# Kernel tuning notes

Hardware: AMD Instinct MI355X
Metric: run time of the kernel (lower is better)

## Reference

```python
import jax, jax.numpy as jnp
import numpy as np

HID = 1024
EMB = 300
VOCAB = 3863
POSE = 514  # autoencoder_vq_components(512) + 2


def gru_step(h, x, Wih, Whh, bih, bhh):
    # PyTorch GRU cell math. x:[B,Din] h:[B,H] Wih:[3H,Din] Whh:[3H,H]
    gi = x @ Wih.T + bih
    gh = h @ Whh.T + bhh
    i_r, i_z, i_n = jnp.split(gi, 3, axis=-1)
    h_r, h_z, h_n = jnp.split(gh, 3, axis=-1)
    r = jax.nn.sigmoid(i_r + h_r)
    z = jax.nn.sigmoid(i_z + h_z)
    n = jnp.tanh(i_n + r * h_n)
    return (1.0 - z) * n + z * h


def setup_inputs() -> dict:
    key = jax.random.key(0)
    ks = jax.random.split(key, 24)
    s_e = 1.0 / np.sqrt(HID)

    def u(k, shape, scale):
        return jax.random.uniform(k, shape, jnp.float32, -scale, scale)

    inp = {
        # encoder embedding + bidirectional (2 single-direction) GRU weights
        "enc_emb": jax.random.normal(ks[0], (VOCAB, EMB), jnp.float32),
        "enc_Wih_f": u(ks[1], (3 * HID, EMB), s_e),
        "enc_Whh_f": u(ks[2], (3 * HID, HID), s_e),
        "enc_bih_f": u(ks[3], (3 * HID,), s_e),
        "enc_bhh_f": u(ks[4], (3 * HID,), s_e),
        "enc_Wih_b": u(ks[5], (3 * HID, EMB), s_e),
        "enc_Whh_b": u(ks[6], (3 * HID, HID), s_e),
        "enc_bih_b": u(ks[7], (3 * HID,), s_e),
        "enc_bhh_b": u(ks[8], (3 * HID,), s_e),
        # decoder embedding, GRU, output projection
        "dec_emb": jax.random.normal(ks[9], (POSE, HID), jnp.float32),
        "dec_Wih": u(ks[10], (3 * HID, HID), s_e),
        "dec_Whh": u(ks[11], (3 * HID, HID), s_e),
        "dec_bih": u(ks[12], (3 * HID,), s_e),
        "dec_bhh": u(ks[13], (3 * HID,), s_e),
        "fc_W": u(ks[14], (POSE, HID), s_e),
        "fc_b": u(ks[15], (POSE,), s_e),
        # forward args
        "in_text": jax.random.randint(ks[16], (128, 64), 0, VOCAB, jnp.int64 if jax.config.jax_enable_x64 else jnp.int32),
        "in_lengths": jax.random.randint(ks[17], (128,), 1, 64),
        "poses": jax.random.randint(ks[18], (128, 90), 0, POSE),
        "vid_indices": jax.random.randint(ks[19], (128,), 0, 128),
    }
    return inp


def reference(enc_emb, enc_Wih_f, enc_Whh_f, enc_bih_f, enc_bhh_f,
              enc_Wih_b, enc_Whh_b, enc_bih_b, enc_bhh_b,
              dec_emb, dec_Wih, dec_Whh, dec_bih, dec_bhh,
              fc_W, fc_b, in_text, in_lengths, poses, vid_indices):
    B = in_text.shape[0]
    x_emb = enc_emb[in_text.T]  # [T_in, B, 300]
    h0 = jnp.zeros((B, HID), dtype=enc_emb.dtype)

    # The torch code feeds a bidirectional GRU one timestep at a time while
    # carrying hidden state, so BOTH directions act as forward recurrences
    # with their own weights.
    def enc_f(h, xt):
        return gru_step(h, xt, enc_Wih_f, enc_Whh_f, enc_bih_f, enc_bhh_f), None

    def enc_b(h, xt):
        return gru_step(h, xt, enc_Wih_b, enc_Whh_b, enc_bih_b, enc_bhh_b), None

    hf, _ = jax.lax.scan(enc_f, h0, x_emb)
    hb, _ = jax.lax.scan(enc_b, h0, x_emb)
    dec_h0 = hf + hb  # encoder_hidden[:1] + encoder_hidden[1:]

    # Teacher-forcing branch: input at step di is poses[max(di-1, 0)].
    pt = poses.T  # [T_out, B]
    dec_idx = jnp.concatenate([pt[:1], pt[:-1]], axis=0)
    dec_x = dec_emb[dec_idx]  # [T_out, B, HID]

    def dec_step(h, xt):
        h = gru_step(h, xt, dec_Wih, dec_Whh, dec_bih, dec_bhh)
        return h, h

    _, hs = jax.lax.scan(dec_step, dec_h0, dec_x)  # [T_out, B, HID]
    out = jnp.einsum('tbh,oh->tbo', hs, fc_W) + fc_b  # [T_out, B, 514]
    return out
```

## Files before the change

kernel.cpp:

```cpp
#include <hip/hip_runtime.h>
#include <hip/hip_bf16.h>

#define HID   1024
#define G3    3072
#define EMB   300
#define EMBP  320
#define VOCAB 3863
#define POSE  514
#define BATCH 128
#define TIN   64
#define TOUT  90
#define BH    (BATCH * HID)
#define NBLK  256

typedef __bf16 bf16x8 __attribute__((ext_vector_type(8)));
typedef float  f32x4  __attribute__((ext_vector_type(4)));
typedef __hip_bfloat16 bhalf;
typedef unsigned long long u64;

#define MFMA(a,b,c) __builtin_amdgcn_mfma_f32_16x16x32_bf16((a),(b),(c),0,0,0)

__device__ __forceinline__ float sigm(float x) { return 1.f / (1.f + __expf(-x)); }
__device__ __forceinline__ float tanh_f(float x) { return 1.f - 2.f / (__expf(2.f * x) + 1.f); }

#define COH_LD(dst, base, imm)                                            \
  asm volatile("global_load_dwordx4 %0, %1, off offset:%2 sc0 sc1"        \
               : "=v"(dst) : "v"(base), "i"(imm))

__device__ __forceinline__ void coh_st_h(bhalf* p, float v) {
  union { bhalf b; unsigned short s; } u;
  u.b = __float2bfloat16(v);
  __hip_atomic_store((unsigned short*)p, u.s, __ATOMIC_RELAXED, __HIP_MEMORY_SCOPE_AGENT);
}
__device__ __forceinline__ void coh_st_f(float* p, float v) {
  __hip_atomic_store(p, v, __ATOMIC_RELAXED, __HIP_MEMORY_SCOPE_AGENT);
}
__device__ __forceinline__ float coh_ld_f(const float* p) {
  return __hip_atomic_load((const float*)p, __ATOMIC_RELAXED, __HIP_MEMORY_SCOPE_AGENT);
}

__device__ __forceinline__ void gbar(unsigned* bar, unsigned tgt) {
  __syncthreads();
  if (threadIdx.x == 0) {
    __hip_atomic_fetch_add(bar, 1u, __ATOMIC_RELEASE, __HIP_MEMORY_SCOPE_AGENT);
    while (__hip_atomic_load(bar, __ATOMIC_RELAXED, __HIP_MEMORY_SCOPE_AGENT) < tgt)
      __builtin_amdgcn_s_sleep(1);
  }
  __syncthreads();
  asm volatile("" ::: "memory");
}

__global__ void k_zerobar(unsigned* p) {
  int i = blockIdx.x * 256 + threadIdx.x;
  if (i < 1024)
    __hip_atomic_store(p + i, 0u, __ATOMIC_RELAXED, __HIP_MEMORY_SCOPE_AGENT);
}

__global__ __launch_bounds__(256) void k_convert(const float* __restrict__ src,
        bhalf* __restrict__ dst, int rows_in, int cols_in, int cols_out, int total) {
  int i = blockIdx.x * 256 + threadIdx.x;
  if (i >= total) return;
  int r = i / cols_out, c = i - r * cols_out;
  float v = (r < rows_in && c < cols_in) ? src[(size_t)r * cols_in + c] : 0.f;
  dst[i] = __float2bfloat16(v);
}

__global__ __launch_bounds__(256) void k_pack(const float* __restrict__ whh,
                                              bhalf* __restrict__ dst) {
  int i = blockIdx.x * 256 + threadIdx.x;
  if (i >= G3 * HID) return;
  int k  = i & (HID - 1);
  int rp = i >> 10;
  int jg  = rp / 48;
  int rem = rp - jg * 48;
  int g = rem >> 4, jl = rem & 15;
  int j = (jg << 4) + jl;
  dst[i] = __float2bfloat16(whh[(size_t)((g << 10) + j) * HID + k]);
}

template<int OUTBF>
__global__ __launch_bounds__(256) void k_gemm(
    const bhalf* __restrict__ A, const bhalf* __restrict__ B,
    const float* __restrict__ bias, float* __restrict__ Cf, bhalf* __restrict__ Cb,
    int M, int K, int Nstore) {
  int gx = gridDim.x;
  int nwg = gx * gridDim.y;
  int orig = blockIdx.y * gx + blockIdx.x;
  int xcd = orig & 7, sl = orig >> 3;
  int qq = nwg >> 3, rr = nwg & 7;
  int nbid = (xcd < rr ? xcd * (qq + 1) : rr * (qq + 1) + (xcd - rr) * qq) + sl;
  int bx = nbid % gx, by = nbid / gx;

  int tid = threadIdx.x;
  int l = tid & 63, w = tid >> 6;
  int q = l >> 4, jl = l & 15;
  int n0 = bx * 32;
  int m0 = by * 128 + w * 32;
  int ar0 = m0 + jl;       if (ar0 >= M) ar0 = M - 1;
  int ar1 = m0 + 16 + jl;  if (ar1 >= M) ar1 = M - 1;
  const bhalf* pa0 = A + (size_t)ar0 * K + q * 8;
  const bhalf* pa1 = A + (size_t)ar1 * K + q * 8;
  const bhalf* pb0 = B + (size_t)(n0 + jl) * K + q * 8;
  const bhalf* pb1 = B + (size_t)(n0 + 16 + jl) * K + q * 8;
  f32x4 acc[2][2] = {};
#pragma unroll 4
  for (int kc = 0; kc < K; kc += 32) {
    bf16x8 a0 = *(const bf16x8*)(pa0 + kc);
    bf16x8 a1 = *(const bf16x8*)(pa1 + kc);
    bf16x8 b0 = *(const bf16x8*)(pb0 + kc);
    bf16x8 b1 = *(const bf16x8*)(pb1 + kc);
    acc[0][0] = MFMA(a0, b0, acc[0][0]);
    acc[0][1] = MFMA(a0, b1, acc[0][1]);
    acc[1][0] = MFMA(a1, b0, acc[1][0]);
    acc[1][1] = MFMA(a1, b1, acc[1][1]);
  }
#pragma unroll
  for (int sub = 0; sub < 2; ++sub)
#pragma unroll
    for (int ns = 0; ns < 2; ++ns)
#pragma unroll
      for (int reg = 0; reg < 4; ++reg) {
        int row = m0 + sub * 16 + q * 4 + reg;
        int col = n0 + ns * 16 + jl;
        if (row < M && col < Nstore) {
          float v = acc[sub][ns][reg] + bias[col];
          if (OUTBF) Cb[(size_t)row * Nstore + col] = __float2bfloat16(v);
          else       Cf[(size_t)row * Nstore + col] = v;
        }
      }
}

struct SeqArgs {
  const bhalf *packF, *packB, *packD;
  const bhalf *tabF, *tabB, *tabD;
  const float *bhhF, *bhhB, *bhhD;
  const int *in_text, *poses;
  bhalf *hb0F, *hb1F, *hb0B, *hb1B;
  float *hfinF, *hfinB;
  bhalf *h0bf;
  bhalf *hs;
  unsigned *barF, *barE, *barD;
};

__device__ __forceinline__ void load_w(char* wlds, const bhalf* wsrc, int tid) {
  for (int it = tid; it < 6144; it += 256) {
    int row = it >> 7, c8 = it & 127;
    int off = (row * 1024 + c8 * 8) * 2;
    *(bf16x8*)(wlds + (off ^ ((row & 7) << 4))) =
        *(const bf16x8*)(wsrc + row * 1024 + c8 * 8);
  }
}

__device__ __forceinline__ bf16x8 ldsB(const char* wlds, int row, int kcol) {
  int off = (row * 1024 + kcol) * 2;
  return *(const bf16x8*)(wlds + (off ^ ((row & 7) << 4)));
}

__global__ __launch_bounds__(256) __attribute__((amdgpu_waves_per_eu(1, 1)))
void k_seq(SeqArgs A) {
  __shared__ char  wlds[96 * 1024];
  __shared__ f32x4 part[3][4][3][64];
  int tid = threadIdx.x;
  int l = tid & 63, w = tid >> 6;
  int q = l >> 4, jl = l & 15;
  int bid = blockIdx.x;
  int kbase = w * 256;

  int dir = bid >> 7;
  int mg  = (bid >> 6) & 1;
  int dom = bid >> 6;
  int jb  = bid & 63;
  int m0  = mg * 64;
  int j   = jb * 16 + jl;
  const bhalf* Bp  = dir ? A.packB : A.packF;
  const bhalf* tab = dir ? A.tabB  : A.tabF;
  const float* bhh = dir ? A.bhhB  : A.bhhF;
  bhalf* hpp0 = dir ? A.hb0B : A.hb0F;
  bhalf* hpp1 = dir ? A.hb1B : A.hb1F;
  unsigned* myE = A.barE + (size_t)dom * 32;
  float bhr = bhh[j], bhz = bhh[HID + j], bhn = bhh[2 * HID + j];

  load_w(wlds, Bp + (size_t)jb * 48 * 1024, tid);

  float hreg[4] = {};
#pragma unroll
  for (int reg = 0; reg < 4; ++reg)
    coh_st_h(&hpp0[(size_t)(m0 + w * 16 + q * 4 + reg) * HID + j], 0.f);
  gbar(A.barF, NBLK);

  unsigned et = 0;
  for (int t = 0; t < TIN; ++t) {
    const bhalf* hcur = (t & 1) ? hpp1 : hpp0;
    bhalf*       hnxt = (t & 1) ? hpp0 : hpp1;
    float gir[4], giz[4], gin[4];
#pragma unroll
    for (int reg = 0; reg < 4; ++reg) {
      int m = m0 + w * 16 + q * 4 + reg;
      int tok = A.in_text[m * TIN + t];
      const bhalf* gi = tab + (size_t)tok * G3;
      gir[reg] = __bfloat162float(gi[j]);
      giz[reg] = __bfloat162float(gi[HID + j]);
      gin[reg] = __bfloat162float(gi[2 * HID + j]);
    }
    bf16x8 a0_[8], a1_[8], a2_[8], a3_[8];
    {
      const char* pm0 = (const char*)(hcur + (size_t)(m0 + jl) * HID + kbase + q * 8);
      const char* pm1 = pm0 + 16 * HID * 2;
      const char* pm2 = pm0 + 32 * HID * 2;
      const char* pm3 = pm0 + 48 * HID * 2;
#pragma unroll
      for (int i = 0; i < 8; ++i) {
        COH_LD(a0_[i], pm0, i * 64);
        COH_LD(a1_[i], pm1, i * 64);
        COH_LD(a2_[i], pm2, i * 64);
        COH_LD(a3_[i], pm3, i * 64);
      }
    }
    asm volatile("s_waitcnt vmcnt(0)" ::: "memory");
    __builtin_amdgcn_sched_barrier(0);
    f32x4 acc[4][3] = {};
#pragma unroll
    for (int i = 0; i < 8; ++i) {
      bf16x8 b0 = ldsB(wlds,      jl, kbase + i * 32 + q * 8);
      bf16x8 b1 = ldsB(wlds, 16 + jl, kbase + i * 32 + q * 8);
      bf16x8 b2 = ldsB(wlds, 32 + jl, kbase + i * 32 + q * 8);
      acc[0][0] = MFMA(a0_[i], b0, acc[0][0]);
      acc[0][1] = MFMA(a0_[i], b1, acc[0][1]);
      acc[0][2] = MFMA(a0_[i], b2, acc[0][2]);
      acc[1][0] = MFMA(a1_[i], b0, acc[1][0]);
      acc[1][1] = MFMA(a1_[i], b1, acc[1][1]);
      acc[1][2] = MFMA(a1_[i], b2, acc[1][2]);
      acc[2][0] = MFMA(a2_[i], b0, acc[2][0]);
      acc[2][1] = MFMA(a2_[i], b1, acc[2][1]);
      acc[2][2] = MFMA(a2_[i], b2, acc[2][2]);
      acc[3][0] = MFMA(a3_[i], b0, acc[3][0]);
      acc[3][1] = MFMA(a3_[i], b1, acc[3][1]);
      acc[3][2] = MFMA(a3_[i], b2, acc[3][2]);
    }
#pragma unroll
    for (int mt = 0; mt < 4; ++mt) {
      if (mt != w) {
        int wi = w - (w > mt ? 1 : 0);
        part[wi][mt][0][l] = acc[mt][0];
        part[wi][mt][1][l] = acc[mt][1];
        part[wi][mt][2][l] = acc[mt][2];
      }
    }
    __syncthreads();
    f32x4 f0 = {}, f1 = {}, f2 = {};
#pragma unroll
    for (int mt = 0; mt < 4; ++mt)
      if (mt == w) { f0 = acc[mt][0]; f1 = acc[mt][1]; f2 = acc[mt][2]; }
#pragma unroll
    for (int s = 0; s < 3; ++s) {
      f0 += part[s][w][0][l]; f1 += part[s][w][1][l]; f2 += part[s][w][2][l];
    }
#pragma unroll
    for (int reg = 0; reg < 4; ++reg) {
      float r = sigm(gir[reg] + f0[reg] + bhr);
      float z = sigm(giz[reg] + f1[reg] + bhz);
      float n = tanh_f(gin[reg] + r * (f2[reg] + bhn));
      float hv = (1.f - z) * n + z * hreg[reg];
      hreg[reg] = hv;
      coh_st_h(&hnxt[(size_t)(m0 + w * 16 + q * 4 + reg) * HID + j], hv);
    }
    et += 64;
    if (t < TIN - 1) gbar(myE, et);
  }

  {
    float* hfin = dir ? A.hfinB : A.hfinF;
#pragma unroll
    for (int reg = 0; reg < 4; ++reg)
      coh_st_f(&hfin[(size_t)(m0 + w * 16 + q * 4 + reg) * HID + j], hreg[reg]);
  }
  gbar(A.barF, 2 * NBLK);

  int dom2 = bid >> 6;
  int jb2  = bid & 63;
  int m20  = dom2 * 32;
  int j2   = jb2 * 16 + jl;
  unsigned* myD = A.barD + (size_t)dom2 * 32;
  float b2r = A.bhhD[j2], b2z = A.bhhD[HID + j2], b2n = A.bhhD[2 * HID + j2];

  load_w(wlds, A.packD + (size_t)jb2 * 48 * 1024, tid);

  float hreg4[4];
  if (w < 2) {
#pragma unroll
    for (int reg = 0; reg < 4; ++reg) {
      int m = m20 + w * 16 + q * 4 + reg;
      float s = coh_ld_f(&A.hfinF[(size_t)m * HID + j2]) +
                coh_ld_f(&A.hfinB[(size_t)m * HID + j2]);
      hreg4[reg] = s;
      coh_st_h(&A.h0bf[(size_t)m * HID + j2], s);
    }
  }
  unsigned dt = 64;
  gbar(myD, dt);

  for (int t = 0; t < TOUT; ++t) {
    const bhalf* Asrc = t ? (A.hs + (size_t)(t - 1) * BH) : A.h0bf;
    int pt = t ? t - 1 : 0;
    float gir[4], giz[4], gin[4];
    if (w < 2) {
#pragma unroll
      for (int reg = 0; reg < 4; ++reg) {
        int m = m20 + w * 16 + q * 4 + reg;
        int tok = A.poses[m * TOUT + pt];
        const bhalf* gi = A.tabD + (size_t)tok * G3;
        gir[reg] = __bfloat162float(gi[j2]);
        giz[reg] = __bfloat162float(gi[HID + j2]);
        gin[reg] = __bfloat162float(gi[2 * HID + j2]);
      }
    }
    bf16x8 a0_[8], a1_[8];
    {
      const char* pm0 = (const char*)(Asrc + (size_t)(m20 + jl) * HID + kbase + q * 8);
      const char* pm1 = pm0 + 16 * HID * 2;
#pragma unroll
      for (int i = 0; i < 8; ++i) {
        COH_LD(a0_[i], pm0, i * 64);
        COH_LD(a1_[i], pm1, i * 64);
      }
    }
    asm volatile("s_waitcnt vmcnt(0)" ::: "memory");
    __builtin_amdgcn_sched_barrier(0);
    f32x4 acc[2][3] = {};
#pragma unroll
    for (int i = 0; i < 8; ++i) {
      bf16x8 b0 = ldsB(wlds,      jl, kbase + i * 32 + q * 8);
      bf16x8 b1 = ldsB(wlds, 16 + jl, kbase + i * 32 + q * 8);
      bf16x8 b2 = ldsB(wlds, 32 + jl, kbase + i * 32 + q * 8);
      acc[0][0] = MFMA(a0_[i], b0, acc[0][0]);
      acc[0][1] = MFMA(a0_[i], b1, acc[0][1]);
      acc[0][2] = MFMA(a0_[i], b2, acc[0][2]);
      acc[1][0] = MFMA(a1_[i], b0, acc[1][0]);
      acc[1][1] = MFMA(a1_[i], b1, acc[1][1]);
      acc[1][2] = MFMA(a1_[i], b2, acc[1][2]);
    }
#pragma unroll
    for (int mt = 0; mt < 2; ++mt) {
      if (mt != w) {
        int wi = w - (w > mt ? 1 : 0);
        part[wi][mt][0][l] = acc[mt][0];
        part[wi][mt][1][l] = acc[mt][1];
        part[wi][mt][2][l] = acc[mt][2];
      }
    }
    __syncthreads();
    if (w < 2) {
      f32x4 f0 = {}, f1 = {}, f2 = {};
#pragma unroll
      for (int mt = 0; mt < 2; ++mt)
        if (mt == w) { f0 = acc[mt][0]; f1 = acc[mt][1]; f2 = acc[mt][2]; }
#pragma unroll
      for (int s = 0; s < 3; ++s) {
        f0 += part[s][w][0][l]; f1 += part[s][w][1][l]; f2 += part[s][w][2][l];
      }
      bhalf* hout = A.hs + (size_t)t * BH;
#pragma unroll
      for (int reg = 0; reg < 4; ++reg) {
        float r = sigm(gir[reg] + f0[reg] + b2r);
        float z = sigm(giz[reg] + f1[reg] + b2z);
        float n = tanh_f(gin[reg] + r * (f2[reg] + b2n));
        float hv = (1.f - z) * n + z * hreg4[reg];
        hreg4[reg] = hv;
        coh_st_h(&hout[(size_t)(m20 + w * 16 + q * 4 + reg) * HID + j2], hv);
      }
    }
    dt += 64;
    if (t < TOUT - 1) gbar(myD, dt);
  }
}

extern "C" void kernel_launch(void* const* d_in, const int* in_sizes, int n_in,
                              void* d_out, int out_size, void* d_ws, size_t ws_size,
                              hipStream_t stream) {
  const float* enc_emb   = (const float*)d_in[0];
  const float* enc_Wih_f = (const float*)d_in[1];
  const float* enc_Whh_f = (const float*)d_in[2];
  const float* enc_bih_f = (const float*)d_in[3];
  const float* enc_bhh_f = (const float*)d_in[4];
  const float* enc_Wih_b = (const float*)d_in[5];
  const float* enc_Whh_b = (const float*)d_in[6];
  const float* enc_bih_b = (const float*)d_in[7];
  const float* enc_bhh_b = (const float*)d_in[8];
  const float* dec_emb   = (const float*)d_in[9];
  const float* dec_Wih   = (const float*)d_in[10];
  const float* dec_Whh   = (const float*)d_in[11];
  const float* dec_bih   = (const float*)d_in[12];
  const float* dec_bhh   = (const float*)d_in[13];
  const float* fc_W      = (const float*)d_in[14];
  const float* fc_b      = (const float*)d_in[15];
  const int*   in_text   = (const int*)d_in[16];
  const int*   poses     = (const int*)d_in[18];
  float* out = (float*)d_out;

  char* p = (char*)d_ws;
  auto alloc = [&](size_t n) { char* r = p; p += (n + 255) & ~(size_t)255; return r; };
  bhalf* tabF  = (bhalf*)alloc((size_t)VOCAB * G3 * 2);
  bhalf* tabB  = (bhalf*)alloc((size_t)VOCAB * G3 * 2);
  bhalf* tabD  = (bhalf*)alloc((size_t)POSE * G3 * 2);
  bhalf* hb0F  = (bhalf*)alloc(BH * 2);
  bhalf* hb1F  = (bhalf*)alloc(BH * 2);
  bhalf* hb0B  = (bhalf*)alloc(BH * 2);
  bhalf* hb1B  = (bhalf*)alloc(BH * 2);
  float* hfinF = (float*)alloc(BH * 4);
  float* hfinB = (float*)alloc(BH * 4);
  bhalf* h0bf  = (bhalf*)alloc(BH * 2);
  bhalf* hs    = (bhalf*)alloc((size_t)TOUT * BH * 2);
  bhalf* embbf = (bhalf*)alloc((size_t)VOCAB * EMBP * 2);
  bhalf* wihF  = (bhalf*)alloc((size_t)G3 * EMBP * 2);
  bhalf* wihB  = (bhalf*)alloc((size_t)G3 * EMBP * 2);
  bhalf* dembbf= (bhalf*)alloc((size_t)POSE * HID * 2);
  bhalf* dwih  = (bhalf*)alloc((size_t)G3 * HID * 2);
  bhalf* fcw   = (bhalf*)alloc((size_t)544 * HID * 2);
  bhalf* packF = (bhalf*)alloc((size_t)G3 * HID * 2);
  bhalf* packB = (bhalf*)alloc((size_t)G3 * HID * 2);
  bhalf* packD = (bhalf*)alloc((size_t)G3 * HID * 2);
  unsigned* bars = (unsigned*)alloc(4096);
  unsigned* barF = bars;
  unsigned* barE = bars + 32;
  unsigned* barD = bars + 32 + 4 * 32;

  auto cgrid = [](int total) { return dim3((total + 255) / 256); };

  k_zerobar<<<dim3(4), 256, 0, stream>>>(bars);
  k_convert<<<cgrid(VOCAB * EMBP), 256, 0, stream>>>(enc_emb, embbf, VOCAB, EMB, EMBP, VOCAB * EMBP);
  k_convert<<<cgrid(G3 * EMBP),   256, 0, stream>>>(enc_Wih_f, wihF, G3, EMB, EMBP, G3 * EMBP);
  k_convert<<<cgrid(G3 * EMBP),   256, 0, stream>>>(enc_Wih_b, wihB, G3, EMB, EMBP, G3 * EMBP);
  k_convert<<<cgrid(POSE * HID),  256, 0, stream>>>(dec_emb, dembbf, POSE, HID, HID, POSE * HID);
  k_convert<<<cgrid(G3 * HID),    256, 0, stream>>>(dec_Wih, dwih, G3, HID, HID, G3 * HID);
  k_convert<<<cgrid(544 * HID),   256, 0, stream>>>(fc_W, fcw, POSE, HID, HID, 544 * HID);
  k_pack<<<cgrid(G3 * HID), 256, 0, stream>>>(enc_Whh_f, packF);
  k_pack<<<cgrid(G3 * HID), 256, 0, stream>>>(enc_Whh_b, packB);
  k_pack<<<cgrid(G3 * HID), 256, 0, stream>>>(dec_Whh, packD);

  k_gemm<1><<<dim3(96, 31), 256, 0, stream>>>(embbf, wihF, enc_bih_f, nullptr, tabF, VOCAB, EMBP, G3);
  k_gemm<1><<<dim3(96, 31), 256, 0, stream>>>(embbf, wihB, enc_bih_b, nullptr, tabB, VOCAB, EMBP, G3);
  k_gemm<1><<<dim3(96, 5),  256, 0, stream>>>(dembbf, dwih, dec_bih, nullptr, tabD, POSE, HID, G3);

  SeqArgs sa;
  sa.packF = packF; sa.packB = packB; sa.packD = packD;
  sa.tabF = tabF; sa.tabB = tabB; sa.tabD = tabD;
  sa.bhhF = enc_bhh_f; sa.bhhB = enc_bhh_b; sa.bhhD = dec_bhh;
  sa.in_text = in_text; sa.poses = poses;
  sa.hb0F = hb0F; sa.hb1F = hb1F; sa.hb0B = hb0B; sa.hb1B = hb1B;
  sa.hfinF = hfinF; sa.hfinB = hfinB; sa.h0bf = h0bf; sa.hs = hs;
  sa.barF = barF; sa.barE = barE; sa.barD = barD;
  k_seq<<<dim3(NBLK), dim3(256), 0, stream>>>(sa);

  k_gemm<0><<<dim3(17, 90), 256, 0, stream>>>(hs, fcw, fc_b, out, nullptr, TOUT * BATCH, HID, POSE);
}
```

Baseline: 1.874 ms.

## Prefetch next-step input gate rows and split vmcnt waits across MFMA chunks

Moves the token and input-gate table gathers off the critical path by loading the next timestep's values during the current step's MFMA loop. It also replaces the single full vmcnt(0) wait with staged waits, so MFMA work on early hidden-state chunks can begin while later loads are still in flight. This adds hand-counted outstanding-load bookkeeping, and a wrong count would break correctness. It also adds a full drain after the grid barrier each step.

```diff
diff --git a/kernel.cpp b/kernel.cpp
--- a/kernel.cpp
+++ b/kernel.cpp
@@ -26,6 +26,11 @@
 #define COH_LD(dst, base, imm)                                            \
   asm volatile("global_load_dwordx4 %0, %1, off offset:%2 sc0 sc1"        \
                : "=v"(dst) : "v"(base), "i"(imm))
+#define TOK_LD(dst, addr)                                                 \
+  asm volatile("global_load_dword %0, %1, off" : "=v"(dst) : "v"(addr))
+#define GI_LD(dst, addr, imm)                                             \
+  asm volatile("global_load_ushort %0, %1, off offset:%2"                 \
+               : "=v"(dst) : "v"(addr), "i"(imm))
 
 __device__ __forceinline__ void coh_st_h(bhalf* p, float v) {
   union { bhalf b; unsigned short s; } u;
@@ -156,6 +161,38 @@
   return *(const bf16x8*)(wlds + (off ^ ((row & 7) << 4)));
 }
 
+#define ENC_CHUNK(i) {                                                        \
+  bf16x8 b0 = ldsB(wlds,      jl, kbase + (i) * 32 + q * 8);                  \
+  bf16x8 b1 = ldsB(wlds, 16 + jl, kbase + (i) * 32 + q * 8);                  \
+  bf16x8 b2 = ldsB(wlds, 32 + jl, kbase + (i) * 32 + q * 8);                  \
+  acc[0][0] = MFMA(a0_[i], b0, acc[0][0]);                                    \
+  acc[0][1] = MFMA(a0_[i], b1, acc[0][1]);                                    \
+  acc[0][2] = MFMA(a0_[i], b2, acc[0][2]);                                    \
+  acc[1][0] = MFMA(a1_[i], b0, acc[1][0]);                                    \
+  acc[1][1] = MFMA(a1_[i], b1, acc[1][1]);                                    \
+  acc[1][2] = MFMA(a1_[i], b2, acc[1][2]);                                    \
+  acc[2][0] = MFMA(a2_[i], b0, acc[2][0]);                                    \
+  acc[2][1] = MFMA(a2_[i], b1, acc[2][1]);                                    \
+  acc[2][2] = MFMA(a2_[i], b2, acc[2][2]);                                    \
+  acc[3][0] = MFMA(a3_[i], b0, acc[3][0]);                                    \
+  acc[3][1] = MFMA(a3_[i], b1, acc[3][1]);                                    \
+  acc[3][2] = MFMA(a3_[i], b2, acc[3][2]); }
+
+#define DEC_CHUNK(i) {                                                        \
+  bf16x8 b0 = ldsB(wlds,      jl, kbase + (i) * 32 + q * 8);                  \
+  bf16x8 b1 = ldsB(wlds, 16 + jl, kbase + (i) * 32 + q * 8);                  \
+  bf16x8 b2 = ldsB(wlds, 32 + jl, kbase + (i) * 32 + q * 8);                  \
+  acc[0][0] = MFMA(a0_[i], b0, acc[0][0]);                                    \
+  acc[0][1] = MFMA(a0_[i], b1, acc[0][1]);                                    \
+  acc[0][2] = MFMA(a0_[i], b2, acc[0][2]);                                    \
+  acc[1][0] = MFMA(a1_[i], b0, acc[1][0]);                                    \
+  acc[1][1] = MFMA(a1_[i], b1, acc[1][1]);                                    \
+  acc[1][2] = MFMA(a1_[i], b2, acc[1][2]); }
+
+#define VMWAIT(N)                                                             \
+  asm volatile("s_waitcnt vmcnt(" #N ")" ::: "memory");                       \
+  __builtin_amdgcn_sched_barrier(0);
+
 __global__ __launch_bounds__(256) __attribute__((amdgpu_waves_per_eu(1, 1)))
 void k_seq(SeqArgs A) {
   __shared__ char  wlds[96 * 1024];
@@ -182,6 +219,17 @@
 
   load_w(wlds, Bp + (size_t)jb * 48 * 1024, tid);
 
+  float curR[4], curZ[4], curN[4];
+#pragma unroll
+  for (int reg = 0; reg < 4; ++reg) {
+    int m = m0 + w * 16 + q * 4 + reg;
+    int tok = A.in_text[m * TIN + 0];
+    const bhalf* gi = tab + (size_t)tok * G3;
+    curR[reg] = __bfloat162float(gi[j]);
+    curZ[reg] = __bfloat162float(gi[HID + j]);
+    curN[reg] = __bfloat162float(gi[2 * HID + j]);
+  }
+
   float hreg[4] = {};
 #pragma unroll
   for (int reg = 0; reg < 4; ++reg)
@@ -192,22 +240,19 @@
   for (int t = 0; t < TIN; ++t) {
     const bhalf* hcur = (t & 1) ? hpp1 : hpp0;
     bhalf*       hnxt = (t & 1) ? hpp0 : hpp1;
-    float gir[4], giz[4], gin[4];
-#pragma unroll
-    for (int reg = 0; reg < 4; ++reg) {
-      int m = m0 + w * 16 + q * 4 + reg;
-      int tok = A.in_text[m * TIN + t];
-      const bhalf* gi = tab + (size_t)tok * G3;
-      gir[reg] = __bfloat162float(gi[j]);
-      giz[reg] = __bfloat162float(gi[HID + j]);
-      gin[reg] = __bfloat162float(gi[2 * HID + j]);
+    int tn = (t + 1 < TIN) ? t + 1 : t;
+    unsigned tkn[4];
+#pragma unroll
+    for (int reg = 0; reg < 4; ++reg) {
+      const int* ta = A.in_text + (m0 + w * 16 + q * 4 + reg) * TIN + tn;
+      TOK_LD(tkn[reg], ta);
     }
     bf16x8 a0_[8], a1_[8], a2_[8], a3_[8];
     {
       const char* pm0 = (const char*)(hcur + (size_t)(m0 + jl) * HID + kbase + q * 8);
-      const char* pm1 = pm0 + 16 * HID * 2;
-      const char* pm2 = pm0 + 32 * HID * 2;
-      const char* pm3 = pm0 + 48 * HID * 2;
+      const char* pm1 = pm0 + 32768;
+      const char* pm2 = pm0 + 65536;
+      const char* pm3 = pm0 + 98304;
 #pragma unroll
       for (int i = 0; i < 8; ++i) {
         COH_LD(a0_[i], pm0, i * 64);
@@ -216,27 +261,20 @@
         COH_LD(a3_[i], pm3, i * 64);
       }
     }
-    asm volatile("s_waitcnt vmcnt(0)" ::: "memory");
-    __builtin_amdgcn_sched_barrier(0);
     f32x4 acc[4][3] = {};
-#pragma unroll
-    for (int i = 0; i < 8; ++i) {
-      bf16x8 b0 = ldsB(wlds,      jl, kbase + i * 32 + q * 8);
-      bf16x8 b1 = ldsB(wlds, 16 + jl, kbase + i * 32 + q * 8);
-      bf16x8 b2 = ldsB(wlds, 32 + jl, kbase + i * 32 + q * 8);
-      acc[0][0] = MFMA(a0_[i], b0, acc[0][0]);
-      acc[0][1] = MFMA(a0_[i], b1, acc[0][1]);
-      acc[0][2] = MFMA(a0_[i], b2, acc[0][2]);
-      acc[1][0] = MFMA(a1_[i], b0, acc[1][0]);
-      acc[1][1] = MFMA(a1_[i], b1, acc[1][1]);
-      acc[1][2] = MFMA(a1_[i], b2, acc[1][2]);
-      acc[2][0] = MFMA(a2_[i], b0, acc[2][0]);
-      acc[2][1] = MFMA(a2_[i], b1, acc[2][1]);
-      acc[2][2] = MFMA(a2_[i], b2, acc[2][2]);
-      acc[3][0] = MFMA(a3_[i], b0, acc[3][0]);
-      acc[3][1] = MFMA(a3_[i], b1, acc[3][1]);
-      acc[3][2] = MFMA(a3_[i], b2, acc[3][2]);
-    }
+    VMWAIT(24) ENC_CHUNK(0) ENC_CHUNK(1)
+    VMWAIT(16) ENC_CHUNK(2) ENC_CHUNK(3)
+    unsigned gR[4], gZ[4], gN[4];
+#pragma unroll
+    for (int reg = 0; reg < 4; ++reg) {
+      const char* ga  = (const char*)(tab + (size_t)tkn[reg] * G3 + j);
+      const char* ga2 = ga + 4096;
+      GI_LD(gR[reg], ga, 0);
+      GI_LD(gZ[reg], ga, 2048);
+      GI_LD(gN[reg], ga2, 0);
+    }
+    VMWAIT(20) ENC_CHUNK(4) ENC_CHUNK(5)
+    VMWAIT(12) ENC_CHUNK(6) ENC_CHUNK(7)
 #pragma unroll
     for (int mt = 0; mt < 4; ++mt) {
       if (mt != w) {
@@ -257,15 +295,22 @@
     }
 #pragma unroll
     for (int reg = 0; reg < 4; ++reg) {
-      float r = sigm(gir[reg] + f0[reg] + bhr);
-      float z = sigm(giz[reg] + f1[reg] + bhz);
-      float n = tanh_f(gin[reg] + r * (f2[reg] + bhn));
+      float r = sigm(curR[reg] + f0[reg] + bhr);
+      float z = sigm(curZ[reg] + f1[reg] + bhz);
+      float n = tanh_f(curN[reg] + r * (f2[reg] + bhn));
       float hv = (1.f - z) * n + z * hreg[reg];
       hreg[reg] = hv;
       coh_st_h(&hnxt[(size_t)(m0 + w * 16 + q * 4 + reg) * HID + j], hv);
     }
     et += 64;
     if (t < TIN - 1) gbar(myE, et);
+    VMWAIT(0)
+#pragma unroll
+    for (int reg = 0; reg < 4; ++reg) {
+      curR[reg] = __uint_as_float(gR[reg] << 16);
+      curZ[reg] = __uint_as_float(gZ[reg] << 16);
+      curN[reg] = __uint_as_float(gN[reg] << 16);
+    }
   }
 
   {
@@ -285,6 +330,16 @@
 
   load_w(wlds, A.packD + (size_t)jb2 * 48 * 1024, tid);
 
+#pragma unroll
+  for (int reg = 0; reg < 4; ++reg) {
+    int m = m20 + (w & 1) * 16 + q * 4 + reg;
+    int tok = A.poses[m * TOUT + 0];
+    const bhalf* gi = A.tabD + (size_t)tok * G3;
+    curR[reg] = __bfloat162float(gi[j2]);
+    curZ[reg] = __bfloat162float(gi[HID + j2]);
+    curN[reg] = __bfloat162float(gi[2 * HID + j2]);
+  }
+
   float hreg4[4];
   if (w < 2) {
 #pragma unroll
@@ -301,44 +356,37 @@
 
   for (int t = 0; t < TOUT; ++t) {
     const bhalf* Asrc = t ? (A.hs + (size_t)(t - 1) * BH) : A.h0bf;
-    int pt = t ? t - 1 : 0;
-    float gir[4], giz[4], gin[4];
-    if (w < 2) {
-#pragma unroll
-      for (int reg = 0; reg < 4; ++reg) {
-        int m = m20 + w * 16 + q * 4 + reg;
-        int tok = A.poses[m * TOUT + pt];
-        const bhalf* gi = A.tabD + (size_t)tok * G3;
-        gir[reg] = __bfloat162float(gi[j2]);
-        giz[reg] = __bfloat162float(gi[HID + j2]);
-        gin[reg] = __bfloat162float(gi[2 * HID + j2]);
-      }
+    int tnp = (t + 1 < TOUT) ? t : (t - 1);
+    unsigned tkn[4];
+#pragma unroll
+    for (int reg = 0; reg < 4; ++reg) {
+      const int* ta = A.poses + (m20 + (w & 1) * 16 + q * 4 + reg) * TOUT + tnp;
+      TOK_LD(tkn[reg], ta);
     }
     bf16x8 a0_[8], a1_[8];
     {
       const char* pm0 = (const char*)(Asrc + (size_t)(m20 + jl) * HID + kbase + q * 8);
-      const char* pm1 = pm0 + 16 * HID * 2;
+      const char* pm1 = pm0 + 32768;
 #pragma unroll
       for (int i = 0; i < 8; ++i) {
         COH_LD(a0_[i], pm0, i * 64);
         COH_LD(a1_[i], pm1, i * 64);
       }
     }
-    asm volatile("s_waitcnt vmcnt(0)" ::: "memory");
-    __builtin_amdgcn_sched_barrier(0);
     f32x4 acc[2][3] = {};
-#pragma unroll
-    for (int i = 0; i < 8; ++i) {
-      bf16x8 b0 = ldsB(wlds,      jl, kbase + i * 32 + q * 8);
-      bf16x8 b1 = ldsB(wlds, 16 + jl, kbase + i * 32 + q * 8);
-      bf16x8 b2 = ldsB(wlds, 32 + jl, kbase + i * 32 + q * 8);
-      acc[0][0] = MFMA(a0_[i], b0, acc[0][0]);
-      acc[0][1] = MFMA(a0_[i], b1, acc[0][1]);
-      acc[0][2] = MFMA(a0_[i], b2, acc[0][2]);
-      acc[1][0] = MFMA(a1_[i], b0, acc[1][0]);
-      acc[1][1] = MFMA(a1_[i], b1, acc[1][1]);
-      acc[1][2] = MFMA(a1_[i], b2, acc[1][2]);
-    }
+    VMWAIT(12) DEC_CHUNK(0) DEC_CHUNK(1)
+    VMWAIT(8)  DEC_CHUNK(2) DEC_CHUNK(3)
+    unsigned gR[4], gZ[4], gN[4];
+#pragma unroll
+    for (int reg = 0; reg < 4; ++reg) {
+      const char* ga  = (const char*)(A.tabD + (size_t)tkn[reg] * G3 + j2);
+      const char* ga2 = ga + 4096;
+      GI_LD(gR[reg], ga, 0);
+      GI_LD(gZ[reg], ga, 2048);
+      GI_LD(gN[reg], ga2, 0);
+    }
+    VMWAIT(16) DEC_CHUNK(4) DEC_CHUNK(5)
+    VMWAIT(12) DEC_CHUNK(6) DEC_CHUNK(7)
 #pragma unroll
     for (int mt = 0; mt < 2; ++mt) {
       if (mt != w) {
@@ -361,9 +409,9 @@
       bhalf* hout = A.hs + (size_t)t * BH;
 #pragma unroll
       for (int reg = 0; reg < 4; ++reg) {
-        float r = sigm(gir[reg] + f0[reg] + b2r);
-        float z = sigm(giz[reg] + f1[reg] + b2z);
-        float n = tanh_f(gin[reg] + r * (f2[reg] + b2n));
+        float r = sigm(curR[reg] + f0[reg] + b2r);
+        float z = sigm(curZ[reg] + f1[reg] + b2z);
+        float n = tanh_f(curN[reg] + r * (f2[reg] + b2n));
         float hv = (1.f - z) * n + z * hreg4[reg];
         hreg4[reg] = hv;
         coh_st_h(&hout[(size_t)(m20 + w * 16 + q * 4 + reg) * HID + j2], hv);
@@ -371,6 +419,13 @@
     }
     dt += 64;
     if (t < TOUT - 1) gbar(myD, dt);
+    VMWAIT(0)
+#pragma unroll
+    for (int reg = 0; reg < 4; ++reg) {
+      curR[reg] = __uint_as_float(gR[reg] << 16);
+      curZ[reg] = __uint_as_float(gZ[reg] << 16);
+      curN[reg] = __uint_as_float(gN[reg] << 16);
+    }
   }
 }
 
```

Result: slower. 1.941 ms (+3.6%).
